# Kernel optimization log

Measured on AMD Instinct MI355X. Metric: run time of the kernel, lower is better.

Reference implementation:

```python
import jax, jax.numpy as jnp
import numpy as np

K = 3  # hardcoded kNN size in the module

def setup_inputs() -> dict:
    key = jax.random.key(0)
    ks = jax.random.split(key, 8)
    B, M, N, C, NC, OUT = 2, 4096, 8192, 512, 20, 512
    def rn(k, sh, sc=1.0):
        return jax.random.normal(k, sh, dtype=jnp.float32) * sc
    return {
        "src_points": rn(ks[0], (B, M, 3)),
        "tgt_points": rn(ks[1], (B, N, 3)),
        "src_features": rn(ks[2], (B, M, C)),
        # semantic_head: Linear(C,128) -> ReLU -> Linear(128,NC)
        "w_sem1": rn(ks[3], (C, 128), 0.04), "b_sem1": jnp.zeros((128,), jnp.float32),
        "w_sem2": rn(ks[4], (128, NC), 0.08), "b_sem2": jnp.zeros((NC,), jnp.float32),
        # upsample_net: Linear(C+NC,256) -> ReLU -> Linear(256,OUT)
        "w_up1": rn(ks[5], (C + NC, 256), 0.04), "b_up1": jnp.zeros((256,), jnp.float32),
        "w_up2": rn(ks[6], (256, OUT), 0.06), "b_up2": jnp.zeros((OUT,), jnp.float32),
    }

def reference(src_points, tgt_points, src_features,
              w_sem1, b_sem1, w_sem2, b_sem2,
              w_up1, b_up1, w_up2, b_up2):
    # semantic logits per source point: [B, M, NC]
    semantic_logits = jax.nn.relu(src_features @ w_sem1 + b_sem1) @ w_sem2 + b_sem2
    # pairwise euclidean distances tgt->src: [B, N, M]
    d2 = (jnp.sum(tgt_points * tgt_points, -1)[:, :, None]
          + jnp.sum(src_points * src_points, -1)[:, None, :]
          - 2.0 * jnp.einsum('bnd,bmd->bnm', tgt_points, src_points))
    dists = jnp.sqrt(jnp.maximum(d2, 0.0))
    # k smallest distances and their indices
    neg_vals, knn_idx = jax.lax.top_k(-dists, K)   # [B, N, K]
    knn_d = -neg_vals                               # gathered distances, [B, N, K]
    # gather neighbor features / semantics: [B, N, K, C] and [B, N, K, NC]
    knn_features = jax.vmap(lambda f, i: f[i])(src_features, knn_idx)
    knn_semantic = jax.vmap(lambda f, i: f[i])(semantic_logits, knn_idx)
    # inverse-distance softmax weights over the K neighbors
    weights = jax.nn.softmax(-knn_d, axis=-1)                       # [B, N, K]
    semantic_weights = jax.nn.softmax(knn_semantic, axis=-1).mean(axis=2)  # [B, N, NC]
    fused_features = jnp.einsum('bnkd,bnk->bnd', knn_features, weights)    # [B, N, C]
    combined = jnp.concatenate([fused_features, semantic_weights], axis=-1)
    upsampled = jax.nn.relu(combined @ w_up1 + b_up1) @ w_up2 + b_up2      # [B, N, OUT]
    return (upsampled, semantic_logits)
```

## Files before the change

kernel.cpp:

```cpp
#include <hip/hip_runtime.h>
#include <math.h>

#define BB 2
#define MM 4096
#define NN 8192
#define CC 512
#define NC 20
#define OUTD 512
#define H1 128
#define H2 256
#define CIN 532
#define KNN 3
#define SPLIT 16
#define CHUNK (MM / SPLIT)
#define CLEN (CHUNK / 4)

#define RR 32
#define HS 264
#define KT2 8
#define KT1 17

#define RO 16
#define FS 520
#define HS2 136
#define TS 512
#define SKT1 16
#define SKT2 4
#define NSEMB (BB * MM / RO)
#define NKNNB (BB * NN / 256 * SPLIT)

typedef __attribute__((ext_vector_type(8))) short s8;
typedef __attribute__((ext_vector_type(4))) float f4;

__device__ inline unsigned short f2bf(float x) {
    unsigned u = __float_as_uint(x);
    unsigned r = (u + 0x7FFFu + ((u >> 16) & 1u)) >> 16;
    return (unsigned short)r;
}
__device__ inline float bf2fs(short u) {
    return __uint_as_float(((unsigned)(unsigned short)u) << 16);
}

__global__ __launch_bounds__(256) void prep_kernel(
    const float* __restrict__ wu1, const float* __restrict__ wu2,
    const float* __restrict__ ws1, const float* __restrict__ ws2,
    unsigned short* __restrict__ w1p, unsigned short* __restrict__ w2p,
    unsigned short* __restrict__ ws1p, unsigned short* __restrict__ ws2p)
{
    int i = blockIdx.x * 256 + threadIdx.x;
    if (i < KT1 * H2 * 32) {
        int kk = i & 31, n = (i >> 5) & 255, kb = i >> 13;
        int k = kb * 32 + kk;
        w1p[i] = f2bf((k < CIN) ? wu1[(size_t)k * H2 + n] : 0.0f);
    }
    if (i < KT2 * OUTD * 32) {
        int kk = i & 31, n = (i >> 5) & 511, kb = i >> 14;
        int k = kb * 32 + kk;
        w2p[i] = f2bf(wu2[(size_t)k * OUTD + n]);
    }
    if (i < SKT1 * H1 * 32) {
        int kk = i & 31, n = (i >> 5) & 127, kb = i >> 12;
        int k = kb * 32 + kk;
        ws1p[i] = f2bf(ws1[(size_t)k * H1 + n]);
    }
    if (i < SKT2 * 32 * 32) {
        int kk = i & 31, n = (i >> 5) & 31, kb = i >> 10;
        int k = kb * 32 + kk;
        ws2p[i] = f2bf((n < NC) ? ws2[(size_t)k * NC + n] : 0.0f);
    }
}

__global__ __launch_bounds__(256) void phase1_kernel(
    const float* __restrict__ feat,
    const unsigned short* __restrict__ ws1p, const unsigned short* __restrict__ ws2p,
    const unsigned short* __restrict__ w1p,
    const float* __restrict__ b1s, const float* __restrict__ b2s,
    float* __restrict__ logits_out, unsigned short* __restrict__ T,
    const float* __restrict__ srcp, const float* __restrict__ tgtp,
    float* __restrict__ pd2, unsigned short* __restrict__ pidx)
{
    __shared__ __align__(16) char smem[40512];
    const int tid = threadIdx.x;
    const int bx = blockIdx.x;

    if (bx < NSEMB) {
        unsigned short* sfeat = (unsigned short*)smem;
        unsigned short* Tst   = (unsigned short*)(smem + 16640);
        unsigned short* shid  = (unsigned short*)(smem + 33024);
        float*          slg   = (float*)(smem + 37376);
        unsigned short* pP    = (unsigned short*)(smem + 39488);
        const int row0 = bx * RO;
        const int lane = tid & 63;
        const int wv = tid >> 6;
        const int l15 = lane & 15;
        const int quad = lane >> 4;

        {
            const int r = tid >> 4, p = tid & 15;
            const float4* fr = (const float4*)(feat + (size_t)(row0 + r) * CC);
#pragma unroll
            for (int j = 0; j < 8; ++j) {
                int c4 = j * 16 + p;
                float4 a = fr[c4];
                ushort4 s;
                s.x = f2bf(a.x); s.y = f2bf(a.y); s.z = f2bf(a.z); s.w = f2bf(a.w);
                *(ushort4*)&sfeat[r * FS + c4 * 4] = s;
            }
        }
        __syncthreads();

        {
            f4 asem[2], ah[4];
#pragma unroll
            for (int c = 0; c < 2; ++c) asem[c] = (f4){0.f, 0.f, 0.f, 0.f};
#pragma unroll
            for (int c = 0; c < 4; ++c) ah[c] = (f4){0.f, 0.f, 0.f, 0.f};
            for (int kb = 0; kb < SKT1; ++kb) {
                s8 a = *(const s8*)&sfeat[l15 * FS + kb * 32 + quad * 8];
#pragma unroll
                for (int c = 0; c < 2; ++c) {
                    s8 b = *(const s8*)&ws1p[((size_t)(kb * H1 + wv * 32 + c * 16 + l15)) * 32 + quad * 8];
                    asem[c] = __builtin_amdgcn_mfma_f32_16x16x32_bf16(a, b, asem[c], 0, 0, 0);
                }
#pragma unroll
                for (int c = 0; c < 4; ++c) {
                    s8 b = *(const s8*)&w1p[((size_t)(kb * H2 + wv * 64 + c * 16 + l15)) * 32 + quad * 8];
                    ah[c] = __builtin_amdgcn_mfma_f32_16x16x32_bf16(a, b, ah[c], 0, 0, 0);
                }
            }
#pragma unroll
            for (int c = 0; c < 2; ++c) {
                int col = wv * 32 + c * 16 + l15;
                float bias = b1s[col];
#pragma unroll
                for (int i = 0; i < 4; ++i) {
                    int rr = quad * 4 + i;
                    shid[rr * HS2 + col] = f2bf(fmaxf(asem[c][i] + bias, 0.0f));
                }
            }
#pragma unroll
            for (int c = 0; c < 4; ++c) {
                int col = wv * 64 + c * 16 + l15;
#pragma unroll
                for (int i = 0; i < 4; ++i) {
                    int rr = quad * 4 + i;
                    Tst[rr * TS + col] = f2bf(ah[c][i]);
                }
            }
        }
        __syncthreads();

        if (wv < 2) {
            f4 acc = (f4){0.f, 0.f, 0.f, 0.f};
            for (int kb = 0; kb < SKT2; ++kb) {
                s8 a = *(const s8*)&shid[l15 * HS2 + kb * 32 + quad * 8];
                s8 b = *(const s8*)&ws2p[((size_t)(kb * 32 + wv * 16 + l15)) * 32 + quad * 8];
                acc = __builtin_amdgcn_mfma_f32_16x16x32_bf16(a, b, acc, 0, 0, 0);
            }
            int col = wv * 16 + l15;
            float bias = (col < NC) ? b2s[col] : 0.0f;
#pragma unroll
            for (int i = 0; i < 4; ++i) {
                int rr = quad * 4 + i;
                float v = acc[i] + bias;
                slg[rr * 33 + col] = v;
                if (col < NC)
                    logits_out[(size_t)(row0 + rr) * NC + col] = v;
            }
        }
        __syncthreads();

        if (tid < RO) {
            int r = tid;
            float mx = -1e30f;
            for (int nc = 0; nc < NC; ++nc) mx = fmaxf(mx, slg[r * 33 + nc]);
            float s = 0.0f;
            float e[NC];
#pragma unroll
            for (int nc = 0; nc < NC; ++nc) { e[nc] = __expf(slg[r * 33 + nc] - mx); s += e[nc]; }
            float inv = 1.0f / s;
#pragma unroll
            for (int nc = 0; nc < 32; ++nc)
                pP[r * 32 + nc] = (nc < NC) ? f2bf(e[nc] * inv) : 0;
        }
        __syncthreads();

        {
            const int lane2 = tid & 63, wv2 = tid >> 6;
            const int l15b = lane2 & 15, quadb = lane2 >> 4;
            s8 a = *(const s8*)&pP[l15b * 32 + quadb * 8];
#pragma unroll
            for (int c = 0; c < 4; ++c) {
                s8 b = *(const s8*)&w1p[((size_t)(16 * H2 + wv2 * 64 + c * 16 + l15b)) * 32 + quadb * 8];
                f4 acc = (f4){0.f, 0.f, 0.f, 0.f};
                acc = __builtin_amdgcn_mfma_f32_16x16x32_bf16(a, b, acc, 0, 0, 0);
                int col = wv2 * 64 + c * 16 + l15b;
#pragma unroll
                for (int i = 0; i < 4; ++i) {
                    int rr = quadb * 4 + i;
                    Tst[rr * TS + 256 + col] = f2bf(acc[i]);
                }
            }
        }
        __syncthreads();

        {
#pragma unroll
            for (int v = 0; v < 4; ++v) {
                int e = (tid + v * 256) * 8;
                int r = e >> 9, c = e & (TS - 1);
                s8 d = *(const s8*)&Tst[e];
                *(s8*)&T[((size_t)(row0 + r)) * TS + c] = d;
            }
        }
    } else {
        float4* pts = (float4*)smem;
        const int idx = bx - NSEMB;
        const int g = idx & 63;
        const int chunk = idx >> 6;
        const int t = g * 256 + tid;
        const int bu = g >> 5;
        const int mbase = chunk * CHUNK;

        {
            const float* spg = srcp + ((size_t)bu * MM + mbase) * 3;
            float x = spg[tid * 3 + 0];
            float y = spg[tid * 3 + 1];
            float z = spg[tid * 3 + 2];
            pts[tid] = make_float4(x, y, z, x * x + y * y + z * z);
        }
        __syncthreads();

        const float tx = tgtp[(size_t)t * 3 + 0];
        const float ty = tgtp[(size_t)t * 3 + 1];
        const float tz = tgtp[(size_t)t * 3 + 2];
        const float m2x = -2.0f * tx, m2y = -2.0f * ty, m2z = -2.0f * tz;

        float b0[4], b1[4], b2[4];
        int i0[4], i1[4], i2[4];
#pragma unroll
        for (int k = 0; k < 4; ++k) {
            b0[k] = b1[k] = b2[k] = 1e30f;
            i0[k] = i1[k] = i2[k] = 0;
        }

#pragma unroll 2
        for (int m = 0; m < CLEN; ++m) {
#pragma unroll
            for (int k = 0; k < 4; ++k) {
                float4 p = pts[k * CLEN + m];
                float d = fmaf(m2x, p.x, fmaf(m2y, p.y, fmaf(m2z, p.z, p.w)));
                int mi = mbase + k * CLEN + m;
                bool l2 = d < b2[k], l1 = d < b1[k], l0 = d < b0[k];
                b2[k] = l1 ? b1[k] : (l2 ? d : b2[k]); i2[k] = l1 ? i1[k] : (l2 ? mi : i2[k]);
                b1[k] = l0 ? b0[k] : (l1 ? d : b1[k]); i1[k] = l0 ? i0[k] : (l1 ? mi : i1[k]);
                b0[k] = l0 ? d : b0[k];                i0[k] = l0 ? mi : i0[k];
            }
        }
#pragma unroll
        for (int k = 1; k < 4; ++k) {
#pragma unroll
            for (int j = 0; j < 3; ++j) {
                float d = (j == 0) ? b0[k] : (j == 1) ? b1[k] : b2[k];
                int   i = (j == 0) ? i0[k] : (j == 1) ? i1[k] : i2[k];
                bool e2 = d < b2[0], e1 = d < b1[0], e0 = d < b0[0];
                b2[0] = e1 ? b1[0] : (e2 ? d : b2[0]); i2[0] = e1 ? i1[0] : (e2 ? i : i2[0]);
                b1[0] = e0 ? b0[0] : (e1 ? d : b1[0]); i1[0] = e0 ? i0[0] : (e1 ? i : i1[0]);
                b0[0] = e0 ? d : b0[0];                i0[0] = e0 ? i : i0[0];
            }
        }
        size_t o = ((size_t)t * SPLIT + chunk) * KNN;
        pd2[o + 0] = b0[0]; pd2[o + 1] = b1[0]; pd2[o + 2] = b2[0];
        pidx[o + 0] = (unsigned short)i0[0];
        pidx[o + 1] = (unsigned short)i1[0];
        pidx[o + 2] = (unsigned short)i2[0];
    }
}

__global__ __launch_bounds__(256) void up_kernel(
    const unsigned short* __restrict__ T,
    const float* __restrict__ pd2, const unsigned short* __restrict__ pidx,
    const float* __restrict__ tgtp,
    const unsigned short* __restrict__ w2p,
    const float* __restrict__ b1g, const float* __restrict__ b2g,
    float* __restrict__ out)
{
    __shared__ unsigned short hid[RR * HS];
    __shared__ float sg[RR][3];
    __shared__ int   sj[RR][3];
    const int tid = threadIdx.x;
    const int row0 = blockIdx.x * RR;
    const int lane = tid & 63;
    const int wv = tid >> 6;
    const int l15 = lane & 15;
    const int quad = lane >> 4;

    if (tid < RR) {
        int row = row0 + tid;
        float b0 = 1e30f, b1 = 1e30f, b2 = 1e30f;
        int i0 = 0, i1 = 0, i2 = 0;
        size_t base = (size_t)row * SPLIT * KNN;
#pragma unroll
        for (int j = 0; j < SPLIT * KNN; ++j) {
            float d = pd2[base + j];
            int m = pidx[base + j];
            bool l2 = d < b2, l1 = d < b1, l0 = d < b0;
            b2 = l1 ? b1 : (l2 ? d : b2); i2 = l1 ? i1 : (l2 ? m : i2);
            b1 = l0 ? b0 : (l1 ? d : b1); i1 = l0 ? i0 : (l1 ? m : i1);
            b0 = l0 ? d : b0;             i0 = l0 ? m : i0;
        }
        float tx = tgtp[(size_t)row * 3 + 0];
        float ty = tgtp[(size_t)row * 3 + 1];
        float tz = tgtp[(size_t)row * 3 + 2];
        float t2 = tx * tx + ty * ty + tz * tz;
        float d0 = sqrtf(fmaxf(b0 + t2, 0.0f));
        float d1 = sqrtf(fmaxf(b1 + t2, 0.0f));
        float d2v = sqrtf(fmaxf(b2 + t2, 0.0f));
        float e1 = __expf(d0 - d1);
        float e2 = __expf(d0 - d2v);
        float inv = 1.0f / (1.0f + e1 + e2);
        sg[tid][0] = inv; sg[tid][1] = e1 * inv; sg[tid][2] = e2 * inv;
        sj[tid][0] = i0; sj[tid][1] = i1; sj[tid][2] = i2;
    }
    __syncthreads();

    {
        const int r = tid >> 3, p = tid & 7, c0 = p * 32;
        int row = row0 + r;
        size_t bofs = (size_t)(row >> 13) * MM;
        float pre[32];
#pragma unroll
        for (int cc = 0; cc < 32; ++cc) pre[cc] = 0.0f;
#pragma unroll
        for (int k = 0; k < 3; ++k) {
            const unsigned short* Tr = T + (bofs + (size_t)sj[r][k]) * TS;
            float gk = sg[r][k];
#pragma unroll
            for (int v = 0; v < 4; ++v) {
                s8 h = *(const s8*)&Tr[c0 + v * 8];
                s8 g = *(const s8*)&Tr[256 + c0 + v * 8];
#pragma unroll
                for (int e = 0; e < 8; ++e) {
                    pre[v * 8 + e] = fmaf(gk, bf2fs(h[e]), pre[v * 8 + e]);
                    pre[v * 8 + e] = fmaf(1.0f / 3.0f, bf2fs(g[e]), pre[v * 8 + e]);
                }
            }
        }
#pragma unroll
        for (int cc = 0; cc < 32; ++cc) {
            int c = c0 + cc;
            hid[r * HS + c] = f2bf(fmaxf(pre[cc] + b1g[c], 0.0f));
        }
    }
    __syncthreads();

    {
        const int m0 = wv * 128;
        f4 acc2[2][8];
#pragma unroll
        for (int rt = 0; rt < 2; ++rt)
#pragma unroll
            for (int c = 0; c < 8; ++c) acc2[rt][c] = (f4){0.f, 0.f, 0.f, 0.f};
        for (int kb = 0; kb < KT2; ++kb) {
            s8 a0 = *(const s8*)&hid[l15 * HS + kb * 32 + quad * 8];
            s8 a1 = *(const s8*)&hid[(l15 + 16) * HS + kb * 32 + quad * 8];
            s8 bfr[8];
#pragma unroll
            for (int c = 0; c < 8; ++c)
                bfr[c] = *(const s8*)&w2p[((size_t)(kb * OUTD + m0 + c * 16 + l15)) * 32 + quad * 8];
#pragma unroll
            for (int c = 0; c < 8; ++c) {
                acc2[0][c] = __builtin_amdgcn_mfma_f32_16x16x32_bf16(a0, bfr[c], acc2[0][c], 0, 0, 0);
                acc2[1][c] = __builtin_amdgcn_mfma_f32_16x16x32_bf16(a1, bfr[c], acc2[1][c], 0, 0, 0);
            }
        }
#pragma unroll
        for (int c = 0; c < 8; ++c) {
            int ccol = m0 + c * 16 + l15;
            float bias = b2g[ccol];
#pragma unroll
            for (int rt = 0; rt < 2; ++rt)
#pragma unroll
                for (int i = 0; i < 4; ++i) {
                    int rr = rt * 16 + quad * 4 + i;
                    out[(size_t)(row0 + rr) * OUTD + ccol] = acc2[rt][c][i] + bias;
                }
        }
    }
}

extern "C" void kernel_launch(void* const* d_in, const int* in_sizes, int n_in,
                              void* d_out, int out_size, void* d_ws, size_t ws_size,
                              hipStream_t stream) {
    (void)in_sizes; (void)n_in; (void)out_size; (void)ws_size;
    const float* src_points   = (const float*)d_in[0];
    const float* tgt_points   = (const float*)d_in[1];
    const float* src_features = (const float*)d_in[2];
    const float* w_sem1 = (const float*)d_in[3];
    const float* b_sem1 = (const float*)d_in[4];
    const float* w_sem2 = (const float*)d_in[5];
    const float* b_sem2 = (const float*)d_in[6];
    const float* w_up1  = (const float*)d_in[7];
    const float* b_up1  = (const float*)d_in[8];
    const float* w_up2  = (const float*)d_in[9];
    const float* b_up2  = (const float*)d_in[10];

    float* out    = (float*)d_out;
    float* ups    = out;
    float* logits = out + (size_t)BB * NN * OUTD;

    char* w = (char*)d_ws;
    unsigned short* T = (unsigned short*)w;    w += (size_t)BB * MM * TS * 2;
    float* pd2  = (float*)w;                   w += (size_t)BB * NN * SPLIT * KNN * 4;
    unsigned short* pidx = (unsigned short*)w; w += (size_t)BB * NN * SPLIT * KNN * 2;
    unsigned short* w1p  = (unsigned short*)w; w += (size_t)KT1 * H2 * 32 * 2;
    unsigned short* w2p  = (unsigned short*)w; w += (size_t)KT2 * OUTD * 32 * 2;
    unsigned short* ws1p = (unsigned short*)w; w += (size_t)SKT1 * H1 * 32 * 2;
    unsigned short* ws2p = (unsigned short*)w; w += (size_t)SKT2 * 32 * 32 * 2;

    prep_kernel<<<dim3((KT1 * H2 * 32 + 255) / 256), dim3(256), 0, stream>>>(
        w_up1, w_up2, w_sem1, w_sem2, w1p, w2p, ws1p, ws2p);
    phase1_kernel<<<dim3(NSEMB + NKNNB), dim3(256), 0, stream>>>(
        src_features, ws1p, ws2p, w1p, b_sem1, b_sem2, logits, T,
        src_points, tgt_points, pd2, pidx);
    up_kernel<<<dim3(BB * NN / RR), dim3(256), 0, stream>>>(
        T, pd2, pidx, tgt_points, w2p, b_up1, b_up2, ups);
}
```

Baseline: 162.5 us.

## Fuse kNN search into weight-prep kernel, split semantic kernel, double kNN split

The kNN partial search now runs in the same launch as weight packing, and the semantic/T-projection work moves into its own kernel with a smaller shared-memory footprint (sfeat and Tst alias). The source-point split doubles so each block scans a shorter chunk, with a deeper unroll. The up kernel's merge of the per-split partial top-3 lists is parallelised across four threads per row followed by a second merge step. This trades more partial results to write and merge for more parallelism and less per-block serial work, at the cost of different overlap between the semantic and kNN phases.

```diff
diff --git a/kernel.cpp b/kernel.cpp
--- a/kernel.cpp
+++ b/kernel.cpp
@@ -11,7 +11,7 @@
 #define H2 256
 #define CIN 532
 #define KNN 3
-#define SPLIT 16
+#define SPLIT 32
 #define CHUNK (MM / SPLIT)
 #define CLEN (CHUNK / 4)
 
@@ -26,7 +26,8 @@
 #define TS 512
 #define SKT1 16
 #define SKT2 4
-#define NSEMB (BB * MM / RO)
+
+#define NPREP 544
 #define NKNNB (BB * NN / 256 * SPLIT)
 
 typedef __attribute__((ext_vector_type(8))) short s8;
@@ -41,239 +42,242 @@
     return __uint_as_float(((unsigned)(unsigned short)u) << 16);
 }
 
-__global__ __launch_bounds__(256) void prep_kernel(
+__global__ __launch_bounds__(256) void pk_kernel(
     const float* __restrict__ wu1, const float* __restrict__ wu2,
     const float* __restrict__ ws1, const float* __restrict__ ws2,
     unsigned short* __restrict__ w1p, unsigned short* __restrict__ w2p,
-    unsigned short* __restrict__ ws1p, unsigned short* __restrict__ ws2p)
+    unsigned short* __restrict__ ws1p, unsigned short* __restrict__ ws2p,
+    const float* __restrict__ srcp, const float* __restrict__ tgtp,
+    float* __restrict__ pd2, unsigned short* __restrict__ pidx)
 {
-    int i = blockIdx.x * 256 + threadIdx.x;
-    if (i < KT1 * H2 * 32) {
-        int kk = i & 31, n = (i >> 5) & 255, kb = i >> 13;
-        int k = kb * 32 + kk;
-        w1p[i] = f2bf((k < CIN) ? wu1[(size_t)k * H2 + n] : 0.0f);
-    }
-    if (i < KT2 * OUTD * 32) {
-        int kk = i & 31, n = (i >> 5) & 511, kb = i >> 14;
-        int k = kb * 32 + kk;
-        w2p[i] = f2bf(wu2[(size_t)k * OUTD + n]);
-    }
-    if (i < SKT1 * H1 * 32) {
-        int kk = i & 31, n = (i >> 5) & 127, kb = i >> 12;
-        int k = kb * 32 + kk;
-        ws1p[i] = f2bf(ws1[(size_t)k * H1 + n]);
-    }
-    if (i < SKT2 * 32 * 32) {
-        int kk = i & 31, n = (i >> 5) & 31, kb = i >> 10;
-        int k = kb * 32 + kk;
-        ws2p[i] = f2bf((n < NC) ? ws2[(size_t)k * NC + n] : 0.0f);
-    }
-}
-
-__global__ __launch_bounds__(256) void phase1_kernel(
+    __shared__ float4 pts[CHUNK];
+    const int tid = threadIdx.x;
+    const int bx = blockIdx.x;
+
+    if (bx < NPREP) {
+        int i = bx * 256 + tid;
+        if (i < KT1 * H2 * 32) {
+            int kk = i & 31, n = (i >> 5) & 255, kb = i >> 13;
+            int k = kb * 32 + kk;
+            w1p[i] = f2bf((k < CIN) ? wu1[(size_t)k * H2 + n] : 0.0f);
+        }
+        if (i < KT2 * OUTD * 32) {
+            int kk = i & 31, n = (i >> 5) & 511, kb = i >> 14;
+            int k = kb * 32 + kk;
+            w2p[i] = f2bf(wu2[(size_t)k * OUTD + n]);
+        }
+        if (i < SKT1 * H1 * 32) {
+            int kk = i & 31, n = (i >> 5) & 127, kb = i >> 12;
+            int k = kb * 32 + kk;
+            ws1p[i] = f2bf(ws1[(size_t)k * H1 + n]);
+        }
+        if (i < SKT2 * 32 * 32) {
+            int kk = i & 31, n = (i >> 5) & 31, kb = i >> 10;
+            int k = kb * 32 + kk;
+            ws2p[i] = f2bf((n < NC) ? ws2[(size_t)k * NC + n] : 0.0f);
+        }
+        return;
+    }
+
+    const int bx2 = bx - NPREP;
+    const int g = bx2 & 63;
+    const int chunk = bx2 >> 6;
+    const int t = g * 256 + tid;
+    const int bu = g >> 5;
+    const int mbase = chunk * CHUNK;
+
+    if (tid < CHUNK) {
+        const float* spg = srcp + ((size_t)bu * MM + mbase) * 3;
+        float x = spg[tid * 3 + 0];
+        float y = spg[tid * 3 + 1];
+        float z = spg[tid * 3 + 2];
+        pts[tid] = make_float4(x, y, z, x * x + y * y + z * z);
+    }
+    __syncthreads();
+
+    const float tx = tgtp[(size_t)t * 3 + 0];
+    const float ty = tgtp[(size_t)t * 3 + 1];
+    const float tz = tgtp[(size_t)t * 3 + 2];
+    const float m2x = -2.0f * tx, m2y = -2.0f * ty, m2z = -2.0f * tz;
+
+    float b0[4], b1[4], b2[4];
+    int i0[4], i1[4], i2[4];
+#pragma unroll
+    for (int k = 0; k < 4; ++k) {
+        b0[k] = b1[k] = b2[k] = 1e30f;
+        i0[k] = i1[k] = i2[k] = 0;
+    }
+
+#pragma unroll 4
+    for (int m = 0; m < CLEN; ++m) {
+#pragma unroll
+        for (int k = 0; k < 4; ++k) {
+            float4 p = pts[k * CLEN + m];
+            float d = fmaf(m2x, p.x, fmaf(m2y, p.y, fmaf(m2z, p.z, p.w)));
+            int mi = mbase + k * CLEN + m;
+            bool l2 = d < b2[k], l1 = d < b1[k], l0 = d < b0[k];
+            b2[k] = l1 ? b1[k] : (l2 ? d : b2[k]); i2[k] = l1 ? i1[k] : (l2 ? mi : i2[k]);
+            b1[k] = l0 ? b0[k] : (l1 ? d : b1[k]); i1[k] = l0 ? i0[k] : (l1 ? mi : i1[k]);
+            b0[k] = l0 ? d : b0[k];                i0[k] = l0 ? mi : i0[k];
+        }
+    }
+#pragma unroll
+    for (int k = 1; k < 4; ++k) {
+#pragma unroll
+        for (int j = 0; j < 3; ++j) {
+            float d = (j == 0) ? b0[k] : (j == 1) ? b1[k] : b2[k];
+            int   i = (j == 0) ? i0[k] : (j == 1) ? i1[k] : i2[k];
+            bool e2 = d < b2[0], e1 = d < b1[0], e0 = d < b0[0];
+            b2[0] = e1 ? b1[0] : (e2 ? d : b2[0]); i2[0] = e1 ? i1[0] : (e2 ? i : i2[0]);
+            b1[0] = e0 ? b0[0] : (e1 ? d : b1[0]); i1[0] = e0 ? i0[0] : (e1 ? i : i1[0]);
+            b0[0] = e0 ? d : b0[0];                i0[0] = e0 ? i : i0[0];
+        }
+    }
+    size_t o = ((size_t)t * SPLIT + chunk) * KNN;
+    pd2[o + 0] = b0[0]; pd2[o + 1] = b1[0]; pd2[o + 2] = b2[0];
+    pidx[o + 0] = (unsigned short)i0[0];
+    pidx[o + 1] = (unsigned short)i1[0];
+    pidx[o + 2] = (unsigned short)i2[0];
+}
+
+__global__ __launch_bounds__(256) void sem_kernel(
     const float* __restrict__ feat,
     const unsigned short* __restrict__ ws1p, const unsigned short* __restrict__ ws2p,
     const unsigned short* __restrict__ w1p,
     const float* __restrict__ b1s, const float* __restrict__ b2s,
-    float* __restrict__ logits_out, unsigned short* __restrict__ T,
-    const float* __restrict__ srcp, const float* __restrict__ tgtp,
-    float* __restrict__ pd2, unsigned short* __restrict__ pidx)
+    float* __restrict__ logits_out, unsigned short* __restrict__ T)
 {
-    __shared__ __align__(16) char smem[40512];
+    __shared__ __align__(16) char smem[24128];
+    unsigned short* sfeat = (unsigned short*)smem;
+    unsigned short* Tst   = (unsigned short*)smem;
+    unsigned short* shid  = (unsigned short*)(smem + 16640);
+    float*          slg   = (float*)(smem + 20992);
+    unsigned short* pP    = (unsigned short*)(smem + 23104);
     const int tid = threadIdx.x;
-    const int bx = blockIdx.x;
-
-    if (bx < NSEMB) {
-        unsigned short* sfeat = (unsigned short*)smem;
-        unsigned short* Tst   = (unsigned short*)(smem + 16640);
-        unsigned short* shid  = (unsigned short*)(smem + 33024);
-        float*          slg   = (float*)(smem + 37376);
-        unsigned short* pP    = (unsigned short*)(smem + 39488);
-        const int row0 = bx * RO;
-        const int lane = tid & 63;
-        const int wv = tid >> 6;
-        const int l15 = lane & 15;
-        const int quad = lane >> 4;
-
-        {
-            const int r = tid >> 4, p = tid & 15;
-            const float4* fr = (const float4*)(feat + (size_t)(row0 + r) * CC);
-#pragma unroll
-            for (int j = 0; j < 8; ++j) {
-                int c4 = j * 16 + p;
-                float4 a = fr[c4];
-                ushort4 s;
-                s.x = f2bf(a.x); s.y = f2bf(a.y); s.z = f2bf(a.z); s.w = f2bf(a.w);
-                *(ushort4*)&sfeat[r * FS + c4 * 4] = s;
-            }
-        }
-        __syncthreads();
-
-        {
-            f4 asem[2], ah[4];
-#pragma unroll
-            for (int c = 0; c < 2; ++c) asem[c] = (f4){0.f, 0.f, 0.f, 0.f};
-#pragma unroll
-            for (int c = 0; c < 4; ++c) ah[c] = (f4){0.f, 0.f, 0.f, 0.f};
-            for (int kb = 0; kb < SKT1; ++kb) {
-                s8 a = *(const s8*)&sfeat[l15 * FS + kb * 32 + quad * 8];
-#pragma unroll
-                for (int c = 0; c < 2; ++c) {
-                    s8 b = *(const s8*)&ws1p[((size_t)(kb * H1 + wv * 32 + c * 16 + l15)) * 32 + quad * 8];
-                    asem[c] = __builtin_amdgcn_mfma_f32_16x16x32_bf16(a, b, asem[c], 0, 0, 0);
-                }
-#pragma unroll
-                for (int c = 0; c < 4; ++c) {
-                    s8 b = *(const s8*)&w1p[((size_t)(kb * H2 + wv * 64 + c * 16 + l15)) * 32 + quad * 8];
-                    ah[c] = __builtin_amdgcn_mfma_f32_16x16x32_bf16(a, b, ah[c], 0, 0, 0);
-                }
-            }
+    const int row0 = blockIdx.x * RO;
+    const int lane = tid & 63;
+    const int wv = tid >> 6;
+    const int l15 = lane & 15;
+    const int quad = lane >> 4;
+
+    {
+        const int r = tid >> 4, p = tid & 15;
+        const float4* fr = (const float4*)(feat + (size_t)(row0 + r) * CC);
+#pragma unroll
+        for (int j = 0; j < 8; ++j) {
+            int c4 = j * 16 + p;
+            float4 a = fr[c4];
+            ushort4 s;
+            s.x = f2bf(a.x); s.y = f2bf(a.y); s.z = f2bf(a.z); s.w = f2bf(a.w);
+            *(ushort4*)&sfeat[r * FS + c4 * 4] = s;
+        }
+    }
+    __syncthreads();
+
+    f4 asem[2], ah[4];
+    {
+#pragma unroll
+        for (int c = 0; c < 2; ++c) asem[c] = (f4){0.f, 0.f, 0.f, 0.f};
+#pragma unroll
+        for (int c = 0; c < 4; ++c) ah[c] = (f4){0.f, 0.f, 0.f, 0.f};
+        for (int kb = 0; kb < SKT1; ++kb) {
+            s8 a = *(const s8*)&sfeat[l15 * FS + kb * 32 + quad * 8];
 #pragma unroll
             for (int c = 0; c < 2; ++c) {
-                int col = wv * 32 + c * 16 + l15;
-                float bias = b1s[col];
-#pragma unroll
-                for (int i = 0; i < 4; ++i) {
-                    int rr = quad * 4 + i;
-                    shid[rr * HS2 + col] = f2bf(fmaxf(asem[c][i] + bias, 0.0f));
-                }
+                s8 b = *(const s8*)&ws1p[((size_t)(kb * H1 + wv * 32 + c * 16 + l15)) * 32 + quad * 8];
+                asem[c] = __builtin_amdgcn_mfma_f32_16x16x32_bf16(a, b, asem[c], 0, 0, 0);
             }
 #pragma unroll
             for (int c = 0; c < 4; ++c) {
-                int col = wv * 64 + c * 16 + l15;
-#pragma unroll
-                for (int i = 0; i < 4; ++i) {
-                    int rr = quad * 4 + i;
-                    Tst[rr * TS + col] = f2bf(ah[c][i]);
-                }
-            }
-        }
-        __syncthreads();
-
-        if (wv < 2) {
-            f4 acc = (f4){0.f, 0.f, 0.f, 0.f};
-            for (int kb = 0; kb < SKT2; ++kb) {
-                s8 a = *(const s8*)&shid[l15 * HS2 + kb * 32 + quad * 8];
-                s8 b = *(const s8*)&ws2p[((size_t)(kb * 32 + wv * 16 + l15)) * 32 + quad * 8];
-                acc = __builtin_amdgcn_mfma_f32_16x16x32_bf16(a, b, acc, 0, 0, 0);
-            }
-            int col = wv * 16 + l15;
-            float bias = (col < NC) ? b2s[col] : 0.0f;
+                s8 b = *(const s8*)&w1p[((size_t)(kb * H2 + wv * 64 + c * 16 + l15)) * 32 + quad * 8];
+                ah[c] = __builtin_amdgcn_mfma_f32_16x16x32_bf16(a, b, ah[c], 0, 0, 0);
+            }
+        }
+    }
+    __syncthreads();
+    {
+#pragma unroll
+        for (int c = 0; c < 2; ++c) {
+            int col = wv * 32 + c * 16 + l15;
+            float bias = b1s[col];
 #pragma unroll
             for (int i = 0; i < 4; ++i) {
                 int rr = quad * 4 + i;
-                float v = acc[i] + bias;
-                slg[rr * 33 + col] = v;
-                if (col < NC)
-                    logits_out[(size_t)(row0 + rr) * NC + col] = v;
-            }
-        }
-        __syncthreads();
-
-        if (tid < RO) {
-            int r = tid;
-            float mx = -1e30f;
-            for (int nc = 0; nc < NC; ++nc) mx = fmaxf(mx, slg[r * 33 + nc]);
-            float s = 0.0f;
-            float e[NC];
-#pragma unroll
-            for (int nc = 0; nc < NC; ++nc) { e[nc] = __expf(slg[r * 33 + nc] - mx); s += e[nc]; }
-            float inv = 1.0f / s;
-#pragma unroll
-            for (int nc = 0; nc < 32; ++nc)
-                pP[r * 32 + nc] = (nc < NC) ? f2bf(e[nc] * inv) : 0;
-        }
-        __syncthreads();
-
-        {
-            const int lane2 = tid & 63, wv2 = tid >> 6;
-            const int l15b = lane2 & 15, quadb = lane2 >> 4;
-            s8 a = *(const s8*)&pP[l15b * 32 + quadb * 8];
-#pragma unroll
-            for (int c = 0; c < 4; ++c) {
-                s8 b = *(const s8*)&w1p[((size_t)(16 * H2 + wv2 * 64 + c * 16 + l15b)) * 32 + quadb * 8];
-                f4 acc = (f4){0.f, 0.f, 0.f, 0.f};
-                acc = __builtin_amdgcn_mfma_f32_16x16x32_bf16(a, b, acc, 0, 0, 0);
-                int col = wv2 * 64 + c * 16 + l15b;
-#pragma unroll
-                for (int i = 0; i < 4; ++i) {
-                    int rr = quadb * 4 + i;
-                    Tst[rr * TS + 256 + col] = f2bf(acc[i]);
-                }
-            }
-        }
-        __syncthreads();
-
-        {
-#pragma unroll
-            for (int v = 0; v < 4; ++v) {
-                int e = (tid + v * 256) * 8;
-                int r = e >> 9, c = e & (TS - 1);
-                s8 d = *(const s8*)&Tst[e];
-                *(s8*)&T[((size_t)(row0 + r)) * TS + c] = d;
-            }
-        }
-    } else {
-        float4* pts = (float4*)smem;
-        const int idx = bx - NSEMB;
-        const int g = idx & 63;
-        const int chunk = idx >> 6;
-        const int t = g * 256 + tid;
-        const int bu = g >> 5;
-        const int mbase = chunk * CHUNK;
-
-        {
-            const float* spg = srcp + ((size_t)bu * MM + mbase) * 3;
-            float x = spg[tid * 3 + 0];
-            float y = spg[tid * 3 + 1];
-            float z = spg[tid * 3 + 2];
-            pts[tid] = make_float4(x, y, z, x * x + y * y + z * z);
-        }
-        __syncthreads();
-
-        const float tx = tgtp[(size_t)t * 3 + 0];
-        const float ty = tgtp[(size_t)t * 3 + 1];
-        const float tz = tgtp[(size_t)t * 3 + 2];
-        const float m2x = -2.0f * tx, m2y = -2.0f * ty, m2z = -2.0f * tz;
-
-        float b0[4], b1[4], b2[4];
-        int i0[4], i1[4], i2[4];
-#pragma unroll
-        for (int k = 0; k < 4; ++k) {
-            b0[k] = b1[k] = b2[k] = 1e30f;
-            i0[k] = i1[k] = i2[k] = 0;
-        }
-
-#pragma unroll 2
-        for (int m = 0; m < CLEN; ++m) {
-#pragma unroll
-            for (int k = 0; k < 4; ++k) {
-                float4 p = pts[k * CLEN + m];
-                float d = fmaf(m2x, p.x, fmaf(m2y, p.y, fmaf(m2z, p.z, p.w)));
-                int mi = mbase + k * CLEN + m;
-                bool l2 = d < b2[k], l1 = d < b1[k], l0 = d < b0[k];
-                b2[k] = l1 ? b1[k] : (l2 ? d : b2[k]); i2[k] = l1 ? i1[k] : (l2 ? mi : i2[k]);
-                b1[k] = l0 ? b0[k] : (l1 ? d : b1[k]); i1[k] = l0 ? i0[k] : (l1 ? mi : i1[k]);
-                b0[k] = l0 ? d : b0[k];                i0[k] = l0 ? mi : i0[k];
-            }
-        }
-#pragma unroll
-        for (int k = 1; k < 4; ++k) {
-#pragma unroll
-            for (int j = 0; j < 3; ++j) {
-                float d = (j == 0) ? b0[k] : (j == 1) ? b1[k] : b2[k];
-                int   i = (j == 0) ? i0[k] : (j == 1) ? i1[k] : i2[k];
-                bool e2 = d < b2[0], e1 = d < b1[0], e0 = d < b0[0];
-                b2[0] = e1 ? b1[0] : (e2 ? d : b2[0]); i2[0] = e1 ? i1[0] : (e2 ? i : i2[0]);
-                b1[0] = e0 ? b0[0] : (e1 ? d : b1[0]); i1[0] = e0 ? i0[0] : (e1 ? i : i1[0]);
-                b0[0] = e0 ? d : b0[0];                i0[0] = e0 ? i : i0[0];
-            }
-        }
-        size_t o = ((size_t)t * SPLIT + chunk) * KNN;
-        pd2[o + 0] = b0[0]; pd2[o + 1] = b1[0]; pd2[o + 2] = b2[0];
-        pidx[o + 0] = (unsigned short)i0[0];
-        pidx[o + 1] = (unsigned short)i1[0];
-        pidx[o + 2] = (unsigned short)i2[0];
+                shid[rr * HS2 + col] = f2bf(fmaxf(asem[c][i] + bias, 0.0f));
+            }
+        }
+#pragma unroll
+        for (int c = 0; c < 4; ++c) {
+            int col = wv * 64 + c * 16 + l15;
+#pragma unroll
+            for (int i = 0; i < 4; ++i) {
+                int rr = quad * 4 + i;
+                Tst[rr * TS + col] = f2bf(ah[c][i]);
+            }
+        }
+    }
+    __syncthreads();
+
+    if (wv < 2) {
+        f4 acc = (f4){0.f, 0.f, 0.f, 0.f};
+        for (int kb = 0; kb < SKT2; ++kb) {
+            s8 a = *(const s8*)&shid[l15 * HS2 + kb * 32 + quad * 8];
+            s8 b = *(const s8*)&ws2p[((size_t)(kb * 32 + wv * 16 + l15)) * 32 + quad * 8];
+            acc = __builtin_amdgcn_mfma_f32_16x16x32_bf16(a, b, acc, 0, 0, 0);
+        }
+        int col = wv * 16 + l15;
+        float bias = (col < NC) ? b2s[col] : 0.0f;
+#pragma unroll
+        for (int i = 0; i < 4; ++i) {
+            int rr = quad * 4 + i;
+            float v = acc[i] + bias;
+            slg[rr * 33 + col] = v;
+            if (col < NC)
+                logits_out[(size_t)(row0 + rr) * NC + col] = v;
+        }
+    }
+    __syncthreads();
+
+    if (tid < RO) {
+        int r = tid;
+        float mx = -1e30f;
+        for (int nc = 0; nc < NC; ++nc) mx = fmaxf(mx, slg[r * 33 + nc]);
+        float s = 0.0f;
+        float e[NC];
+#pragma unroll
+        for (int nc = 0; nc < NC; ++nc) { e[nc] = __expf(slg[r * 33 + nc] - mx); s += e[nc]; }
+        float inv = 1.0f / s;
+#pragma unroll
+        for (int nc = 0; nc < 32; ++nc)
+            pP[r * 32 + nc] = (nc < NC) ? f2bf(e[nc] * inv) : 0;
+    }
+    __syncthreads();
+
+    {
+        s8 a = *(const s8*)&pP[l15 * 32 + quad * 8];
+#pragma unroll
+        for (int c = 0; c < 4; ++c) {
+            s8 b = *(const s8*)&w1p[((size_t)(16 * H2 + wv * 64 + c * 16 + l15)) * 32 + quad * 8];
+            f4 acc = (f4){0.f, 0.f, 0.f, 0.f};
+            acc = __builtin_amdgcn_mfma_f32_16x16x32_bf16(a, b, acc, 0, 0, 0);
+            int col = wv * 64 + c * 16 + l15;
+#pragma unroll
+            for (int i = 0; i < 4; ++i) {
+                int rr = quad * 4 + i;
+                Tst[rr * TS + 256 + col] = f2bf(acc[i]);
+            }
+        }
+    }
+    __syncthreads();
+
+    {
+#pragma unroll
+        for (int v = 0; v < 4; ++v) {
+            int e = (tid + v * 256) * 8;
+            int r = e >> 9, c = e & (TS - 1);
+            s8 d = *(const s8*)&Tst[e];
+            *(s8*)&T[((size_t)(row0 + r)) * TS + c] = d;
+        }
     }
 }
 
@@ -288,6 +292,8 @@
     __shared__ unsigned short hid[RR * HS];
     __shared__ float sg[RR][3];
     __shared__ int   sj[RR][3];
+    __shared__ float pb[RR][4][3];
+    __shared__ int   pi[RR][4][3];
     const int tid = threadIdx.x;
     const int row0 = blockIdx.x * RR;
     const int lane = tid & 63;
@@ -295,13 +301,14 @@
     const int l15 = lane & 15;
     const int quad = lane >> 4;
 
-    if (tid < RR) {
-        int row = row0 + tid;
+    if (tid < RR * 4) {
+        const int r = tid >> 2, p = tid & 3;
+        int row = row0 + r;
         float b0 = 1e30f, b1 = 1e30f, b2 = 1e30f;
         int i0 = 0, i1 = 0, i2 = 0;
-        size_t base = (size_t)row * SPLIT * KNN;
-#pragma unroll
-        for (int j = 0; j < SPLIT * KNN; ++j) {
+        size_t base = (size_t)row * SPLIT * KNN + (size_t)p * 8 * KNN;
+#pragma unroll
+        for (int j = 0; j < 8 * KNN; ++j) {
             float d = pd2[base + j];
             int m = pidx[base + j];
             bool l2 = d < b2, l1 = d < b1, l0 = d < b0;
@@ -309,6 +316,26 @@
             b1 = l0 ? b0 : (l1 ? d : b1); i1 = l0 ? i0 : (l1 ? m : i1);
             b0 = l0 ? d : b0;             i0 = l0 ? m : i0;
         }
+        pb[r][p][0] = b0; pb[r][p][1] = b1; pb[r][p][2] = b2;
+        pi[r][p][0] = i0; pi[r][p][1] = i1; pi[r][p][2] = i2;
+    }
+    __syncthreads();
+
+    if (tid < RR) {
+        int row = row0 + tid;
+        float b0 = 1e30f, b1 = 1e30f, b2 = 1e30f;
+        int i0 = 0, i1 = 0, i2 = 0;
+#pragma unroll
+        for (int p = 0; p < 4; ++p)
+#pragma unroll
+            for (int j = 0; j < 3; ++j) {
+                float d = pb[tid][p][j];
+                int m = pi[tid][p][j];
+                bool l2 = d < b2, l1 = d < b1, l0 = d < b0;
+                b2 = l1 ? b1 : (l2 ? d : b2); i2 = l1 ? i1 : (l2 ? m : i2);
+                b1 = l0 ? b0 : (l1 ? d : b1); i1 = l0 ? i0 : (l1 ? m : i1);
+                b0 = l0 ? d : b0;             i0 = l0 ? m : i0;
+            }
         float tx = tgtp[(size_t)row * 3 + 0];
         float ty = tgtp[(size_t)row * 3 + 1];
         float tz = tgtp[(size_t)row * 3 + 2];
@@ -418,11 +445,11 @@
     unsigned short* ws1p = (unsigned short*)w; w += (size_t)SKT1 * H1 * 32 * 2;
     unsigned short* ws2p = (unsigned short*)w; w += (size_t)SKT2 * 32 * 32 * 2;
 
-    prep_kernel<<<dim3((KT1 * H2 * 32 + 255) / 256), dim3(256), 0, stream>>>(
-        w_up1, w_up2, w_sem1, w_sem2, w1p, w2p, ws1p, ws2p);
-    phase1_kernel<<<dim3(NSEMB + NKNNB), dim3(256), 0, stream>>>(
-        src_features, ws1p, ws2p, w1p, b_sem1, b_sem2, logits, T,
+    pk_kernel<<<dim3(NPREP + NKNNB), dim3(256), 0, stream>>>(
+        w_up1, w_up2, w_sem1, w_sem2, w1p, w2p, ws1p, ws2p,
         src_points, tgt_points, pd2, pidx);
+    sem_kernel<<<dim3(BB * MM / RO), dim3(256), 0, stream>>>(
+        src_features, ws1p, ws2p, w1p, b_sem1, b_sem2, logits, T);
     up_kernel<<<dim3(BB * NN / RR), dim3(256), 0, stream>>>(
         T, pd2, pidx, tgt_points, w2p, b_up1, b_up2, ups);
 }
```

Result: no change. 165.1 us (+1.6%).
